# Kernel optimization log

Measured on AMD Instinct MI355X. Metric: run time of the kernel, lower is better.

## Reference

```python
import jax, jax.numpy as jnp
import numpy as np

N_NODES = 50000
N_EDGES = 800000
D = 128
BN_EPS = 1e-5

def setup_inputs() -> dict:
    key = jax.random.key(0)
    k1, k2, k3, k4, k5 = jax.random.split(key, 5)
    features = jax.random.normal(k1, (N_NODES, D), dtype=jnp.float32)
    W = jax.random.normal(k2, (D, D), dtype=jnp.float32) * (1.0 / np.sqrt(D))
    b = jax.random.normal(k3, (D,), dtype=jnp.float32) * 0.01
    gamma = jnp.ones((D,), dtype=jnp.float32)
    beta = jnp.zeros((D,), dtype=jnp.float32)
    edge_src = jax.random.randint(k4, (N_EDGES,), 0, N_NODES, dtype=jnp.int32)
    edge_dst = jax.random.randint(k5, (N_EDGES,), 0, N_NODES, dtype=jnp.int32)
    return {"features": features, "W": W, "b": b, "gamma": gamma,
            "beta": beta, "edge_src": edge_src, "edge_dst": edge_dst}

def reference(features, W, b, gamma, beta, edge_src, edge_dst):
    h_in = features
    # in-degrees per node, clamped to >= 1
    degs = jax.ops.segment_sum(jnp.ones_like(edge_dst, dtype=jnp.float32),
                               edge_dst, num_segments=N_NODES)
    norm = jnp.clip(degs, 1.0, None) ** -0.5  # [N]
    norm = norm[:, None]                       # [N, 1]
    # symmetric-norm GCN: scale, copy_src + sum reduce, linear apply, scale
    x = features * norm
    agg = jax.ops.segment_sum(x[edge_src], edge_dst, num_segments=N_NODES)  # [N, D]
    h = agg @ W.T + b
    h = h * norm
    # BatchNorm1d (training-mode math: batch stats over nodes, biased var)
    mean = jnp.mean(h, axis=0)
    var = jnp.mean((h - mean) ** 2, axis=0)
    h = (h - mean) * jax.lax.rsqrt(var + BN_EPS) * gamma + beta
    # ReLU activation, residual; dropout is identity in eval
    h = jax.nn.relu(h)
    h = h_in + h
    return h
```

## Files before the change

kernel.cpp:

```cpp
#include <hip/hip_runtime.h>

#define D 128
#define BN_EPS 1e-5f
#define NPART 8
#define NCHUNK 256
#define CAP 64

typedef __attribute__((ext_vector_type(8))) short short8;
typedef __attribute__((ext_vector_type(4))) float f32x4;

__device__ __forceinline__ unsigned short f2bf(float f) {
    unsigned int x = __float_as_uint(f);
    return (unsigned short)((x + 0x7fffu + ((x >> 16) & 1u)) >> 16);
}

__global__ void k_cast(const float4* __restrict__ inA, ushort4* __restrict__ outA, int n4a,
                       const float4* __restrict__ inB, ushort4* __restrict__ outB, int n4b) {
    int i = blockIdx.x * 256 + threadIdx.x;
    const float4* in; ushort4* out; int k;
    if (i < n4a) { in = inA; out = outA; k = i; }
    else { k = i - n4a; if (k >= n4b) return; in = inB; out = outB; }
    float4 v = in[k];
    ushort4 o;
    o.x = f2bf(v.x); o.y = f2bf(v.y); o.z = f2bf(v.z); o.w = f2bf(v.w);
    out[k] = o;
}

__global__ void p_bucket(const int* __restrict__ src, const int* __restrict__ dst,
                         int* __restrict__ cnt, unsigned short* __restrict__ srcs,
                         int nE, int PS, int CH) {
    int p = blockIdx.x & (NPART - 1);
    int c = blockIdx.x >> 3;
    unsigned lo = (unsigned)(p * PS);
    int e0 = c * CH;
    int e1 = min(e0 + CH, nE);
    for (int e = e0 + threadIdx.x; e < e1; e += 512) {
        int ea = e, eb = e + 256;
        int d0 = dst[ea];
        int d1 = (eb < e1) ? dst[eb] : 0;
        bool a0 = (unsigned)d0 - lo < (unsigned)PS;
        bool a1 = (eb < e1) && ((unsigned)d1 - lo < (unsigned)PS);
        int s0 = a0 ? atomicAdd(&cnt[d0], 1) : CAP;
        int s1 = a1 ? atomicAdd(&cnt[d1], 1) : CAP;
        if (s0 < CAP) srcs[(size_t)d0 * CAP + s0] = (unsigned short)src[ea];
        if (s1 < CAP) srcs[(size_t)d1 * CAP + s1] = (unsigned short)src[eb];
    }
}

template <bool FB>
__global__ __launch_bounds__(256) void k_gather(const int* __restrict__ cnt,
                                                const unsigned short* __restrict__ srcs,
                                                const void* __restrict__ featp,
                                                unsigned int* __restrict__ aggout,
                                                int nN) {
    int node = (blockIdx.x * 256 + threadIdx.x) >> 5;
    if (node >= nN) return;
    int l = threadIdx.x & 31;

    int end = cnt[node];
    if (end > CAP) end = CAP;
    const unsigned short* sl = srcs + (size_t)node * CAP;

    float a0 = 0.0f, a1 = 0.0f, a2 = 0.0f, a3 = 0.0f;
    int i = 0;

    if (FB) {
        const uint2* fb = (const uint2*)featp + l;
        for (; i + 3 < end; i += 4) {
            int s0 = sl[i], s1 = sl[i + 1], s2 = sl[i + 2], s3 = sl[i + 3];
            float n0 = rsqrtf(fmaxf((float)cnt[s0], 1.0f));
            float n1 = rsqrtf(fmaxf((float)cnt[s1], 1.0f));
            float n2 = rsqrtf(fmaxf((float)cnt[s2], 1.0f));
            float n3 = rsqrtf(fmaxf((float)cnt[s3], 1.0f));
            uint2 u0 = fb[(size_t)s0 * 32], u1 = fb[(size_t)s1 * 32];
            uint2 u2 = fb[(size_t)s2 * 32], u3 = fb[(size_t)s3 * 32];
            a0 += __uint_as_float(u0.x << 16) * n0 + __uint_as_float(u1.x << 16) * n1
                + __uint_as_float(u2.x << 16) * n2 + __uint_as_float(u3.x << 16) * n3;
            a1 += __uint_as_float(u0.x & 0xffff0000u) * n0 + __uint_as_float(u1.x & 0xffff0000u) * n1
                + __uint_as_float(u2.x & 0xffff0000u) * n2 + __uint_as_float(u3.x & 0xffff0000u) * n3;
            a2 += __uint_as_float(u0.y << 16) * n0 + __uint_as_float(u1.y << 16) * n1
                + __uint_as_float(u2.y << 16) * n2 + __uint_as_float(u3.y << 16) * n3;
            a3 += __uint_as_float(u0.y & 0xffff0000u) * n0 + __uint_as_float(u1.y & 0xffff0000u) * n1
                + __uint_as_float(u2.y & 0xffff0000u) * n2 + __uint_as_float(u3.y & 0xffff0000u) * n3;
        }
        for (; i < end; ++i) {
            int s = sl[i];
            float n = rsqrtf(fmaxf((float)cnt[s], 1.0f));
            uint2 u = fb[(size_t)s * 32];
            a0 += __uint_as_float(u.x << 16) * n;
            a1 += __uint_as_float(u.x & 0xffff0000u) * n;
            a2 += __uint_as_float(u.y << 16) * n;
            a3 += __uint_as_float(u.y & 0xffff0000u) * n;
        }
    } else {
        const float4* fb = (const float4*)featp + l;
        for (; i + 3 < end; i += 4) {
            int s0 = sl[i], s1 = sl[i + 1], s2 = sl[i + 2], s3 = sl[i + 3];
            float n0 = rsqrtf(fmaxf((float)cnt[s0], 1.0f));
            float n1 = rsqrtf(fmaxf((float)cnt[s1], 1.0f));
            float n2 = rsqrtf(fmaxf((float)cnt[s2], 1.0f));
            float n3 = rsqrtf(fmaxf((float)cnt[s3], 1.0f));
            float4 f0 = fb[(size_t)s0 * 32], f1 = fb[(size_t)s1 * 32];
            float4 f2 = fb[(size_t)s2 * 32], f3 = fb[(size_t)s3 * 32];
            a0 += f0.x * n0 + f1.x * n1 + f2.x * n2 + f3.x * n3;
            a1 += f0.y * n0 + f1.y * n1 + f2.y * n2 + f3.y * n3;
            a2 += f0.z * n0 + f1.z * n1 + f2.z * n2 + f3.z * n3;
            a3 += f0.w * n0 + f1.w * n1 + f2.w * n2 + f3.w * n3;
        }
        for (; i < end; ++i) {
            int s = sl[i];
            float n = rsqrtf(fmaxf((float)cnt[s], 1.0f));
            float4 f = fb[(size_t)s * 32];
            a0 += f.x * n; a1 += f.y * n; a2 += f.z * n; a3 += f.w * n;
        }
    }
    uint2 packed;
    packed.x = (unsigned int)f2bf(a0) | ((unsigned int)f2bf(a1) << 16);
    packed.y = (unsigned int)f2bf(a2) | ((unsigned int)f2bf(a3) << 16);
    ((uint2*)aggout)[(size_t)node * 64 + 32 + l] = packed;
}

__global__ __launch_bounds__(256) void k_gemm(
        const unsigned short* __restrict__ Adata,
        const unsigned short* __restrict__ Wbf,
        const float* __restrict__ b,
        const int* __restrict__ cnt,
        float* __restrict__ h,
        float* __restrict__ colsum, float* __restrict__ colsq,
        int nN) {
    const int tid = threadIdx.x;
    const int lane = tid & 63;
    const int wv = tid >> 6;
    const int wcol0 = wv * 32;
    const int l15 = lane & 15;
    const int lq = lane >> 4;
    const int row0 = blockIdx.x * 64;

    short8 bfrag[2][4];
    #pragma unroll
    for (int ct = 0; ct < 2; ++ct) {
        int n = wcol0 + ct * 16 + l15;
        #pragma unroll
        for (int kc = 0; kc < 4; ++kc)
            bfrag[ct][kc] = *(const short8*)(Wbf + n * 128 + kc * 32 + lq * 8);
    }
    const float bc0 = b[wcol0 + l15], bc1 = b[wcol0 + 16 + l15];

    short8 afrag[4][4];
    #pragma unroll
    for (int rt = 0; rt < 4; ++rt) {
        int arow = row0 + rt * 16 + l15;
        int arc = arow < nN ? arow : (nN - 1);
        #pragma unroll
        for (int kc = 0; kc < 4; ++kc)
            afrag[rt][kc] = *(const short8*)(Adata + (size_t)arc * 256 + 128 + kc * 32 + lq * 8);
    }
    __syncthreads();

    float s1[2] = {0.0f, 0.0f}, s2[2] = {0.0f, 0.0f};

    #pragma unroll
    for (int rt = 0; rt < 4; ++rt) {
        int r0 = row0 + rt * 16;
        f32x4 acc0 = {0.0f, 0.0f, 0.0f, 0.0f};
        f32x4 acc1 = {0.0f, 0.0f, 0.0f, 0.0f};
        #pragma unroll
        for (int kc = 0; kc < 4; ++kc) {
            acc0 = __builtin_amdgcn_mfma_f32_16x16x32_bf16(afrag[rt][kc], bfrag[0][kc], acc0, 0, 0, 0);
            acc1 = __builtin_amdgcn_mfma_f32_16x16x32_bf16(afrag[rt][kc], bfrag[1][kc], acc1, 0, 0, 0);
        }

        #pragma unroll
        for (int reg = 0; reg < 4; ++reg) {
            int row = r0 + lq * 4 + reg;
            if (row < nN) {
                float nm = rsqrtf(fmaxf((float)cnt[row], 1.0f));
                float v0 = (acc0[reg] + bc0) * nm;
                float v1 = (acc1[reg] + bc1) * nm;
                h[(size_t)row * 128 + wcol0 + l15] = v0;
                h[(size_t)row * 128 + wcol0 + 16 + l15] = v1;
                s1[0] += v0; s2[0] += v0 * v0;
                s1[1] += v1; s2[1] += v1 * v1;
            }
        }
    }

    #pragma unroll
    for (int ct = 0; ct < 2; ++ct) {
        s1[ct] += __shfl_xor(s1[ct], 16, 64);
        s1[ct] += __shfl_xor(s1[ct], 32, 64);
        s2[ct] += __shfl_xor(s2[ct], 16, 64);
        s2[ct] += __shfl_xor(s2[ct], 32, 64);
    }
    if (lane < 16) {
        atomicAdd(&colsum[wcol0 + lane], s1[0]);
        atomicAdd(&colsq [wcol0 + lane], s2[0]);
        atomicAdd(&colsum[wcol0 + 16 + lane], s1[1]);
        atomicAdd(&colsq [wcol0 + 16 + lane], s2[1]);
    }
}

__global__ __launch_bounds__(256) void k_bn_out(const float* __restrict__ colsum,
                                                const float* __restrict__ colsq,
                                                const float* __restrict__ gamma,
                                                const float* __restrict__ beta,
                                                float* __restrict__ h,
                                                const float* __restrict__ feat,
                                                float inv_n, int total4) {
    __shared__ float sc[128], sh[128];
    int tid = threadIdx.x;
    if (tid < 128) {
        float mean = colsum[tid] * inv_n;
        float var = colsq[tid] * inv_n - mean * mean;
        float s = gamma[tid] * rsqrtf(var + BN_EPS);
        sc[tid] = s;
        sh[tid] = beta[tid] - mean * s;
    }
    __syncthreads();
    int t = blockIdx.x * 256 + tid;
    if (t >= total4) return;
    int base = t * 4;
    int j = base & 127;
    float4 hv = *(const float4*)(h + base);
    float4 fv = *(const float4*)(feat + base);
    float4 o;
    o.x = fv.x + fmaxf(hv.x * sc[j + 0] + sh[j + 0], 0.0f);
    o.y = fv.y + fmaxf(hv.y * sc[j + 1] + sh[j + 1], 0.0f);
    o.z = fv.z + fmaxf(hv.z * sc[j + 2] + sh[j + 2], 0.0f);
    o.w = fv.w + fmaxf(hv.w * sc[j + 3] + sh[j + 3], 0.0f);
    *(float4*)(h + base) = o;
}

extern "C" void kernel_launch(void* const* d_in, const int* in_sizes, int n_in,
                              void* d_out, int out_size, void* d_ws, size_t ws_size,
                              hipStream_t stream) {
    const float* feat  = (const float*)d_in[0];
    const float* W     = (const float*)d_in[1];
    const float* b     = (const float*)d_in[2];
    const float* gamma = (const float*)d_in[3];
    const float* beta  = (const float*)d_in[4];
    const int* esrc = (const int*)d_in[5];
    const int* edst = (const int*)d_in[6];

    const int nN = in_sizes[0] / D;
    const int nE = in_sizes[5];
    const int PS = (nN + NPART - 1) / NPART;
    const int CH = (nE + NCHUNK - 1) / NCHUNK;

    float* h = (float*)d_out;

    unsigned short* Wbf    = (unsigned short*)d_ws;
    unsigned short* srcs   = Wbf + 128 * 128;
    int*            cnt    = (int*)(srcs + (size_t)nN * CAP);
    float*          colsum = (float*)(cnt + nN);
    float*          colsq  = colsum + 128;
    unsigned short* featbf = (unsigned short*)(colsq + 128);

    size_t need_full = (size_t)((char*)(featbf + (size_t)nN * D) - (char*)d_ws);
    bool useFB = ws_size >= need_full;

    hipMemsetAsync(cnt, 0, ((size_t)nN + 256) * sizeof(int), stream);

    int n4a = 128 * 128 / 4;
    int n4b = useFB ? nN * D / 4 : 0;
    k_cast<<<(n4a + n4b + 255) / 256, 256, 0, stream>>>(
        (const float4*)W, (ushort4*)Wbf, n4a,
        (const float4*)feat, (ushort4*)featbf, n4b);

    p_bucket<<<NPART * NCHUNK, 256, 0, stream>>>(esrc, edst, cnt, srcs, nE, PS, CH);

    int gblocks = (nN * 32 + 255) / 256;
    if (useFB)
        k_gather<true><<<gblocks, 256, 0, stream>>>(cnt, srcs, featbf, (unsigned int*)d_out, nN);
    else
        k_gather<false><<<gblocks, 256, 0, stream>>>(cnt, srcs, feat, (unsigned int*)d_out, nN);

    k_gemm<<<(nN + 63) / 64, 256, 0, stream>>>((const unsigned short*)d_out, Wbf, b, cnt,
                                               h, colsum, colsq, nN);

    int total4 = nN * D / 4;
    k_bn_out<<<(total4 + 255) / 256, 256, 0, stream>>>(colsum, colsq, gamma, beta,
                                                       h, feat, 1.0f / (float)nN, total4);
}
```

Measured before the change: 211.9 us.

## Fuse cast and bucketing kernels, stage GEMM stores through LDS, bucket BN stats

```diff
diff --git a/kernel.cpp b/kernel.cpp
--- a/kernel.cpp
+++ b/kernel.cpp
@@ -5,6 +5,7 @@
 #define NPART 8
 #define NCHUNK 256
 #define CAP 64
+#define NBKT 16
 
 typedef __attribute__((ext_vector_type(8))) short short8;
 typedef __attribute__((ext_vector_type(4))) float f32x4;
@@ -14,36 +15,51 @@
     return (unsigned short)((x + 0x7fffu + ((x >> 16) & 1u)) >> 16);
 }
 
-__global__ void k_cast(const float4* __restrict__ inA, ushort4* __restrict__ outA, int n4a,
-                       const float4* __restrict__ inB, ushort4* __restrict__ outB, int n4b) {
-    int i = blockIdx.x * 256 + threadIdx.x;
-    const float4* in; ushort4* out; int k;
-    if (i < n4a) { in = inA; out = outA; k = i; }
-    else { k = i - n4a; if (k >= n4b) return; in = inB; out = outB; }
-    float4 v = in[k];
-    ushort4 o;
-    o.x = f2bf(v.x); o.y = f2bf(v.y); o.z = f2bf(v.z); o.w = f2bf(v.w);
-    out[k] = o;
-}
-
-__global__ void p_bucket(const int* __restrict__ src, const int* __restrict__ dst,
-                         int* __restrict__ cnt, unsigned short* __restrict__ srcs,
-                         int nE, int PS, int CH) {
-    int p = blockIdx.x & (NPART - 1);
-    int c = blockIdx.x >> 3;
-    unsigned lo = (unsigned)(p * PS);
-    int e0 = c * CH;
-    int e1 = min(e0 + CH, nE);
-    for (int e = e0 + threadIdx.x; e < e1; e += 512) {
-        int ea = e, eb = e + 256;
-        int d0 = dst[ea];
-        int d1 = (eb < e1) ? dst[eb] : 0;
-        bool a0 = (unsigned)d0 - lo < (unsigned)PS;
-        bool a1 = (eb < e1) && ((unsigned)d1 - lo < (unsigned)PS);
-        int s0 = a0 ? atomicAdd(&cnt[d0], 1) : CAP;
-        int s1 = a1 ? atomicAdd(&cnt[d1], 1) : CAP;
-        if (s0 < CAP) srcs[(size_t)d0 * CAP + s0] = (unsigned short)src[ea];
-        if (s1 < CAP) srcs[(size_t)d1 * CAP + s1] = (unsigned short)src[eb];
+__device__ __forceinline__ void atomAddF(float* p, float v) {
+    unsafeAtomicAdd(p, v);
+}
+
+__global__ __launch_bounds__(256) void k_prep(
+        const int* __restrict__ src, const int* __restrict__ dst,
+        int* __restrict__ cnt, unsigned short* __restrict__ srcs,
+        int nE, int PS, int CH,
+        const float4* __restrict__ inA, ushort4* __restrict__ outA, int n4a,
+        const float4* __restrict__ inB, ushort4* __restrict__ outB, int n4b) {
+    int bid = blockIdx.x;
+    if (bid < NPART * NCHUNK) {
+        int p = bid & (NPART - 1);
+        int c = bid >> 3;
+        unsigned lo = (unsigned)(p * PS);
+        int e0 = c * CH;
+        int e1 = min(e0 + CH, nE);
+        for (int e = e0 + (int)threadIdx.x; e < e1; e += 1024) {
+            int ea = e, eb = e + 256, ec = e + 512, ed = e + 768;
+            int d0 = dst[ea];
+            int d1 = (eb < e1) ? dst[eb] : 0;
+            int d2 = (ec < e1) ? dst[ec] : 0;
+            int d3 = (ed < e1) ? dst[ed] : 0;
+            bool a0 = (unsigned)d0 - lo < (unsigned)PS;
+            bool a1 = (eb < e1) && ((unsigned)d1 - lo < (unsigned)PS);
+            bool a2 = (ec < e1) && ((unsigned)d2 - lo < (unsigned)PS);
+            bool a3 = (ed < e1) && ((unsigned)d3 - lo < (unsigned)PS);
+            int s0 = a0 ? atomicAdd(&cnt[d0], 1) : CAP;
+            int s1 = a1 ? atomicAdd(&cnt[d1], 1) : CAP;
+            int s2 = a2 ? atomicAdd(&cnt[d2], 1) : CAP;
+            int s3 = a3 ? atomicAdd(&cnt[d3], 1) : CAP;
+            if (s0 < CAP) srcs[(size_t)d0 * CAP + s0] = (unsigned short)src[ea];
+            if (s1 < CAP) srcs[(size_t)d1 * CAP + s1] = (unsigned short)src[eb];
+            if (s2 < CAP) srcs[(size_t)d2 * CAP + s2] = (unsigned short)src[ec];
+            if (s3 < CAP) srcs[(size_t)d3 * CAP + s3] = (unsigned short)src[ed];
+        }
+    } else {
+        int i = (bid - NPART * NCHUNK) * 256 + threadIdx.x;
+        const float4* in; ushort4* out; int k;
+        if (i < n4a) { in = inA; out = outA; k = i; }
+        else { k = i - n4a; if (k >= n4b) return; in = inB; out = outB; }
+        float4 v = in[k];
+        ushort4 o;
+        o.x = f2bf(v.x); o.y = f2bf(v.y); o.z = f2bf(v.z); o.w = f2bf(v.w);
+        out[k] = o;
     }
 }
 
@@ -126,7 +142,7 @@
         const float* __restrict__ b,
         const int* __restrict__ cnt,
         float* __restrict__ h,
-        float* __restrict__ colsum, float* __restrict__ colsq,
+        float* __restrict__ colpart,
         int nN) {
     const int tid = threadIdx.x;
     const int lane = tid & 63;
@@ -136,6 +152,8 @@
     const int lq = lane >> 4;
     const int row0 = blockIdx.x * 64;
 
+    __shared__ float tp[4][16 * 36];
+
     short8 bfrag[2][4];
     #pragma unroll
     for (int ct = 0; ct < 2; ++ct) {
@@ -158,6 +176,8 @@
     __syncthreads();
 
     float s1[2] = {0.0f, 0.0f}, s2[2] = {0.0f, 0.0f};
+    const int sub = lane & 3;
+    const int r16 = lane >> 2;
 
     #pragma unroll
     for (int rt = 0; rt < 4; ++rt) {
@@ -173,15 +193,25 @@
         #pragma unroll
         for (int reg = 0; reg < 4; ++reg) {
             int row = r0 + lq * 4 + reg;
+            float nm = 0.0f;
+            if (row < nN) nm = rsqrtf(fmaxf((float)cnt[row], 1.0f));
+            float v0 = (acc0[reg] + bc0) * nm;
+            float v1 = (acc1[reg] + bc1) * nm;
+            int lrow = lq * 4 + reg;
+            tp[wv][lrow * 36 + l15]      = v0;
+            tp[wv][lrow * 36 + 16 + l15] = v1;
             if (row < nN) {
-                float nm = rsqrtf(fmaxf((float)cnt[row], 1.0f));
-                float v0 = (acc0[reg] + bc0) * nm;
-                float v1 = (acc1[reg] + bc1) * nm;
-                h[(size_t)row * 128 + wcol0 + l15] = v0;
-                h[(size_t)row * 128 + wcol0 + 16 + l15] = v1;
                 s1[0] += v0; s2[0] += v0 * v0;
                 s1[1] += v1; s2[1] += v1 * v1;
             }
+        }
+        int row = r0 + r16;
+        if (row < nN) {
+            float4 t0 = *(const float4*)&tp[wv][r16 * 36 + sub * 4];
+            float4 t1 = *(const float4*)&tp[wv][r16 * 36 + 16 + sub * 4];
+            size_t base = (size_t)row * 128 + wcol0 + sub * 4;
+            *(float4*)(h + base) = t0;
+            *(float4*)(h + base + 16) = t1;
         }
     }
 
@@ -192,16 +222,16 @@
         s2[ct] += __shfl_xor(s2[ct], 16, 64);
         s2[ct] += __shfl_xor(s2[ct], 32, 64);
     }
+    const int bkt = blockIdx.x & (NBKT - 1);
     if (lane < 16) {
-        atomicAdd(&colsum[wcol0 + lane], s1[0]);
-        atomicAdd(&colsq [wcol0 + lane], s2[0]);
-        atomicAdd(&colsum[wcol0 + 16 + lane], s1[1]);
-        atomicAdd(&colsq [wcol0 + 16 + lane], s2[1]);
-    }
-}
-
-__global__ __launch_bounds__(256) void k_bn_out(const float* __restrict__ colsum,
-                                                const float* __restrict__ colsq,
+        atomAddF(&colpart[(wcol0 + lane) * NBKT + bkt], s1[0]);
+        atomAddF(&colpart[(128 + wcol0 + lane) * NBKT + bkt], s2[0]);
+        atomAddF(&colpart[(wcol0 + 16 + lane) * NBKT + bkt], s1[1]);
+        atomAddF(&colpart[(128 + wcol0 + 16 + lane) * NBKT + bkt], s2[1]);
+    }
+}
+
+__global__ __launch_bounds__(256) void k_bn_out(const float* __restrict__ colpart,
                                                 const float* __restrict__ gamma,
                                                 const float* __restrict__ beta,
                                                 float* __restrict__ h,
@@ -210,11 +240,17 @@
     __shared__ float sc[128], sh[128];
     int tid = threadIdx.x;
     if (tid < 128) {
-        float mean = colsum[tid] * inv_n;
-        float var = colsq[tid] * inv_n - mean * mean;
-        float s = gamma[tid] * rsqrtf(var + BN_EPS);
-        sc[tid] = s;
-        sh[tid] = beta[tid] - mean * s;
+        float s = 0.0f, q = 0.0f;
+        #pragma unroll
+        for (int j = 0; j < NBKT; ++j) {
+            s += colpart[tid * NBKT + j];
+            q += colpart[(128 + tid) * NBKT + j];
+        }
+        float mean = s * inv_n;
+        float var = q * inv_n - mean * mean;
+        float scv = gamma[tid] * rsqrtf(var + BN_EPS);
+        sc[tid] = scv;
+        sh[tid] = beta[tid] - mean * scv;
     }
     __syncthreads();
     int t = blockIdx.x * 256 + tid;
@@ -252,22 +288,21 @@
     unsigned short* Wbf    = (unsigned short*)d_ws;
     unsigned short* srcs   = Wbf + 128 * 128;
     int*            cnt    = (int*)(srcs + (size_t)nN * CAP);
-    float*          colsum = (float*)(cnt + nN);
-    float*          colsq  = colsum + 128;
-    unsigned short* featbf = (unsigned short*)(colsq + 128);
+    float*          colpart= (float*)(cnt + nN);
+    unsigned short* featbf = (unsigned short*)(colpart + 256 * NBKT);
 
     size_t need_full = (size_t)((char*)(featbf + (size_t)nN * D) - (char*)d_ws);
     bool useFB = ws_size >= need_full;
 
-    hipMemsetAsync(cnt, 0, ((size_t)nN + 256) * sizeof(int), stream);
+    hipMemsetAsync(cnt, 0, ((size_t)nN + 256 * NBKT + 64) * sizeof(int), stream);
 
     int n4a = 128 * 128 / 4;
     int n4b = useFB ? nN * D / 4 : 0;
-    k_cast<<<(n4a + n4b + 255) / 256, 256, 0, stream>>>(
+    int castBlocks = (n4a + n4b + 255) / 256;
+    k_prep<<<NPART * NCHUNK + castBlocks, 256, 0, stream>>>(
+        esrc, edst, cnt, srcs, nE, PS, CH,
         (const float4*)W, (ushort4*)Wbf, n4a,
         (const float4*)feat, (ushort4*)featbf, n4b);
-
-    p_bucket<<<NPART * NCHUNK, 256, 0, stream>>>(esrc, edst, cnt, srcs, nE, PS, CH);
 
     int gblocks = (nN * 32 + 255) / 256;
     if (useFB)
@@ -275,10 +310,13 @@
     else
         k_gather<false><<<gblocks, 256, 0, stream>>>(cnt, srcs, feat, (unsigned int*)d_out, nN);
 
-    k_gemm<<<(nN + 63) / 64, 256, 0, stream>>>((const unsigned short*)d_out, Wbf, b, cnt,
-                                               h, colsum, colsq, nN);
+    int gb = (nN + 63) / 64;
+    float inv_n = 1.0f / (float)nN;
+
+    k_gemm<<<gb, 256, 0, stream>>>((const unsigned short*)d_out, Wbf, b, cnt,
+                                   h, colpart, nN);
 
     int total4 = nN * D / 4;
-    k_bn_out<<<(total4 + 255) / 256, 256, 0, stream>>>(colsum, colsq, gamma, beta,
-                                                       h, feat, 1.0f / (float)nN, total4);
-}
+    k_bn_out<<<(total4 + 255) / 256, 256, 0, stream>>>(colpart, gamma, beta,
+                                                       h, feat, inv_n, total4);
+}
```

Measured after the change: 210.5 us. No clear change (-0.7%).
